# Kernel optimization log

Measured on AMD Instinct MI355X. Metric: run time of the kernel, lower is better.

Reference implementation:

```python
import jax, jax.numpy as jnp
import numpy as np

B, S, D, H = 2, 2048, 1024, 16
DK = D // H  # 64
SQRT_DK = DK ** 0.5
NEG = -1e9


def setup_inputs() -> dict:
    key = jax.random.key(0)
    ks = jax.random.split(key, 7)
    scale = 1.0 / np.sqrt(D)
    return {
        "x": jax.random.normal(ks[0], (B, S, D), jnp.float32),
        "encoder_output": jax.random.normal(ks[1], (B, S, D), jnp.float32),
        "mask": jax.random.randint(ks[2], (B, S), 0, 2, jnp.int32),
        "WQ": jax.random.normal(ks[3], (D, D), jnp.float32) * scale,
        "WK": jax.random.normal(ks[4], (D, D), jnp.float32) * scale,
        "WV": jax.random.normal(ks[5], (D, D), jnp.float32) * scale,
        "WO": jax.random.normal(ks[6], (D, D), jnp.float32) * scale,
    }


def reference(x, encoder_output, mask, WQ, WK, WV, WO):
    b, s, d = x.shape
    # project and split heads: (b, h, s, dk)
    q = (x @ WQ).reshape(b, s, H, DK).transpose(0, 2, 1, 3)
    k = (encoder_output @ WK).reshape(b, s, H, DK).transpose(0, 2, 1, 3)
    v = (encoder_output @ WV).reshape(b, s, H, DK).transpose(0, 2, 1, 3)
    # scores: (b, h, s_q, s_k)
    scores = jnp.einsum('bhqd,bhkd->bhqk', q, k) / SQRT_DK
    # future mask (strict upper triangle) + padding mask broadcast over key dim
    future = jnp.triu(jnp.ones((s, s), jnp.int32), 1)  # (s, s)
    m = mask[:, None, :, None] + future[None, None, :, :]  # (b, 1->h, s_q, s_k)
    scores = jnp.where(m != 0, NEG, scores)
    attn = jax.nn.softmax(scores, axis=-1)
    # context: (b, s, h, dk) -> (b, s, d)
    ctx = jnp.einsum('bhqk,bhkd->bqhd', attn, v).reshape(b, s, d)
    return ctx @ WO
```

## Files before the change

### kernel.cpp

```cpp
#include <hip/hip_runtime.h>
#include <hip/hip_bf16.h>

constexpr int B = 2, S = 2048, D = 1024, H = 16, DK = 64;
constexpr int M = B * S;
constexpr float LOG2E = 1.44269504088896f;
constexpr float NEGBIG = -3.0e38f;
constexpr float QSCALE = 0.125f * LOG2E;

using short8 = __attribute__((ext_vector_type(8))) short;
using short4v = __attribute__((ext_vector_type(4))) short;
using f32x4 = __attribute__((ext_vector_type(4))) float;

#define GLOBAL_AS __attribute__((address_space(1)))
#define LDS_AS __attribute__((address_space(3)))

__device__ __forceinline__ void gll16(const void* g, void* l) {
  __builtin_amdgcn_global_load_lds((const GLOBAL_AS void*)g, (LDS_AS void*)l, 16, 0, 0);
}

__device__ __forceinline__ short f2bf(float f) {
  __hip_bfloat16 h = __float2bfloat16(f);
  short s;
  __builtin_memcpy(&s, &h, 2);
  return s;
}
__device__ __forceinline__ unsigned pack2bf(float a, float b) {
  return (unsigned)(unsigned short)f2bf(a) | ((unsigned)(unsigned short)f2bf(b) << 16);
}

__global__ __launch_bounds__(256) void prep_kernel(const float* __restrict__ x,
                                                   const float* __restrict__ enc,
                                                   const float* __restrict__ W0,
                                                   const float* __restrict__ W1,
                                                   const float* __restrict__ W2,
                                                   const float* __restrict__ W3,
                                                   short* __restrict__ xb,
                                                   short* __restrict__ encb,
                                                   short* __restrict__ Wt) {
  __shared__ float t[64][65];
  const int bx = blockIdx.x;
  if (bx < 8192) {
    const float4* src = (const float4*)((bx & 4096) ? enc : x);
    short4v* dst = (short4v*)((bx & 4096) ? encb : xb);
    const int i = (bx & 4095) * 256 + threadIdx.x;
    const float4 v = src[i];
    short4v o;
    o[0] = f2bf(v.x); o[1] = f2bf(v.y); o[2] = f2bf(v.z); o[3] = f2bf(v.w);
    dst[i] = o;
  } else {
    const int idx = bx - 8192;
    const int z = idx >> 8, rem = idx & 255;
    const float* W = z == 0 ? W0 : z == 1 ? W1 : z == 2 ? W2 : W3;
    short* dstw = Wt + (size_t)z * D * D;
    const int n0 = (rem & 15) * 64, k0 = (rem >> 4) * 64;
    const int lx = threadIdx.x & 63, ly = threadIdx.x >> 6;
    #pragma unroll
    for (int r = 0; r < 64; r += 4)
      t[r + ly][lx] = W[(size_t)(k0 + r + ly) * D + n0 + lx];
    __syncthreads();
    #pragma unroll
    for (int r = 0; r < 64; r += 4)
      dstw[(size_t)(n0 + r + ly) * D + k0 + lx] = f2bf(t[lx][r + ly]);
  }
}

__global__ __launch_bounds__(512, 2) void gemm_qkv_kernel(const short* __restrict__ A0,
                                                          const short* __restrict__ A1,
                                                          const short* __restrict__ Wts,
                                                          short* __restrict__ Cv,
                                                          float* __restrict__ vsum) {
  __shared__ char AsL[65536];
  __shared__ char BsL[65536];
  const int z = blockIdx.z;
  const short* __restrict__ A = z ? A1 : A0;
  const short* __restrict__ Bt = Wts + (size_t)z * D * D;
  const float oscale = (z == 0) ? QSCALE : 1.0f;

  const int tid = threadIdx.x;
  const int lane = tid & 63, wid = tid >> 6;
  const int l15 = lane & 15, lg = lane >> 4;
  const int row0 = blockIdx.x * 256, col0 = blockIdx.y * 256;
  const int wm = wid >> 2, wn = wid & 3;
  f32x4 acc[8][4] = {};

  auto stageH = [&](int mat, int sbuf, int half, int tile) {
    const short* src = mat ? Bt : A;
    const int base0 = mat ? col0 : row0;
    char* dst = (mat ? BsL : AsL) + sbuf * 32768 + half * 16384;
    const int k0 = tile * 64;
    #pragma unroll
    for (int it = 0; it < 2; ++it) {
      const int c = tid + it * 512;
      const int row = c & 127, kc = c >> 7;
      gll16(&src[(size_t)(base0 + half * 128 + row) * D + k0 + kc * 8],
            dst + kc * 2048 + row * 16);
    }
  };

#define PHASE(RBUF, MH, NH, DOSTAGE, SMAT, SBUF, SH, STILE, VM)                            \
  do {                                                                                     \
    short8 af_[4][2], bv_[2][2];                                                           \
    const char* ab_ = AsL + (RBUF) * 32768 + (MH) * 16384;                                 \
    const char* bb_ = BsL + (RBUF) * 32768 + (NH) * 16384;                                 \
    _Pragma("unroll") for (int m16 = 0; m16 < 4; ++m16)                                    \
        _Pragma("unroll") for (int ks = 0; ks < 2; ++ks)                                   \
            af_[m16][ks] = *(const short8*)(ab_ + (ks * 4 + lg) * 2048 +                   \
                                            (wm * 64 + m16 * 16 + l15) * 16);              \
    _Pragma("unroll") for (int n16 = 0; n16 < 2; ++n16)                                    \
        _Pragma("unroll") for (int ks = 0; ks < 2; ++ks)                                   \
            bv_[n16][ks] = *(const short8*)(bb_ + (ks * 4 + lg) * 2048 +                   \
                                            (wn * 32 + n16 * 16 + l15) * 16);              \
    if (DOSTAGE) stageH((SMAT), (SBUF), (SH), (STILE));                                    \
    __builtin_amdgcn_s_barrier();                                                          \
    asm volatile("s_waitcnt lgkmcnt(0)" ::: "memory");                                     \
    __builtin_amdgcn_sched_barrier(0);                                                     \
    __builtin_amdgcn_s_setprio(1);                                                         \
    _Pragma("unroll") for (int m16 = 0; m16 < 4; ++m16)                                    \
        _Pragma("unroll") for (int n16 = 0; n16 < 2; ++n16)                                \
            _Pragma("unroll") for (int ks = 0; ks < 2; ++ks)                               \
                acc[(MH) * 4 + m16][(NH) * 2 + n16] =                                      \
                    __builtin_amdgcn_mfma_f32_16x16x32_bf16(                               \
                        af_[m16][ks], bv_[n16][ks], acc[(MH) * 4 + m16][(NH) * 2 + n16],   \
                        0, 0, 0);                                                          \
    __builtin_amdgcn_s_setprio(0);                                                         \
    if ((VM) == 4) asm volatile("s_waitcnt vmcnt(4)" ::: "memory");                        \
    else if ((VM) == 0) asm volatile("s_waitcnt vmcnt(0)" ::: "memory");                   \
    __builtin_amdgcn_s_barrier();                                                          \
    __builtin_amdgcn_sched_barrier(0);                                                     \
  } while (0)

  stageH(0, 0, 0, 0);
  stageH(1, 0, 0, 0);
  stageH(0, 0, 1, 0);
  stageH(1, 0, 1, 0);
  stageH(0, 1, 0, 1);
  stageH(1, 1, 0, 1);
  asm volatile("s_waitcnt vmcnt(4)" ::: "memory");
  __builtin_amdgcn_s_barrier();
  __builtin_amdgcn_sched_barrier(0);

  #pragma unroll 1
  for (int i = 0; i < 8; ++i) {
    const int tb = 2 * i + 1, ta2 = 2 * i + 2, tb2 = 2 * i + 3;
    const bool pre = (i < 7);
    const int vm = pre ? 4 : 0;
    PHASE(0, 0, 0, true, 0, 1, 1, tb, -1);
    PHASE(0, 0, 1, true, 1, 1, 1, tb, -1);
    PHASE(0, 1, 0, pre, 0, 0, 0, ta2, -1);
    PHASE(0, 1, 1, pre, 1, 0, 0, ta2, vm);
    PHASE(1, 0, 0, pre, 0, 0, 1, ta2, -1);
    PHASE(1, 0, 1, pre, 1, 0, 1, ta2, -1);
    PHASE(1, 1, 0, pre, 0, 1, 0, tb2, -1);
    PHASE(1, 1, 1, pre, 1, 1, 0, tb2, vm);
  }
#undef PHASE

  #pragma unroll
  for (int mh = 0; mh < 2; ++mh)
    #pragma unroll
    for (int m16 = 0; m16 < 4; ++m16)
      #pragma unroll
      for (int r = 0; r < 4; ++r) {
        const int row = row0 + mh * 128 + wm * 64 + m16 * 16 + 4 * lg + r;
        #pragma unroll
        for (int nh = 0; nh < 2; ++nh)
          #pragma unroll
          for (int n16 = 0; n16 < 2; ++n16) {
            const int col = col0 + nh * 128 + wn * 32 + n16 * 16 + l15;
            Cv[(size_t)z * M * D + (size_t)row * D + col] =
                f2bf(acc[mh * 4 + m16][nh * 2 + n16][r] * oscale);
          }
      }
  if (z == 2) {
    const int bidx = row0 >> 11;
    #pragma unroll
    for (int nh = 0; nh < 2; ++nh)
      #pragma unroll
      for (int n16 = 0; n16 < 2; ++n16) {
        float s = 0.f;
        #pragma unroll
        for (int mh = 0; mh < 2; ++mh)
          #pragma unroll
          for (int m16 = 0; m16 < 4; ++m16) {
            const f32x4 a4 = acc[mh * 4 + m16][nh * 2 + n16];
            s += a4[0] + a4[1] + a4[2] + a4[3];
          }
        s += __shfl_xor(s, 16);
        s += __shfl_xor(s, 32);
        if (lg == 0)
          atomicAdd(&vsum[(size_t)bidx * D + col0 + nh * 128 + wn * 32 + n16 * 16 + l15], s);
      }
  }
}

__global__ __launch_bounds__(256) void gemmO_kernel(const short* __restrict__ A,
                                                    const short* __restrict__ Bt,
                                                    float* __restrict__ C) {
  __shared__ short As[2][4][128][8];
  __shared__ short Bs[2][4][64][8];
  const int tid = threadIdx.x;
  const int lane = tid & 63, wid = tid >> 6;
  const int l15 = lane & 15, lg = lane >> 4;
  const int row0 = blockIdx.x * 128, col0 = blockIdx.y * 64;
  const int wm = wid >> 1, wn = wid & 1;
  f32x4 acc[4][2] = {};

  auto stage = [&](int k0, int nb) {
    #pragma unroll
    for (int it = 0; it < 2; ++it) {
      const int c = tid + it * 256;
      const int row = c & 127, kc2 = c >> 7;
      gll16(&A[(size_t)(row0 + row) * D + k0 + kc2 * 8],
            (char*)As + nb * 8192 + (wid * 64 + it * 256) * 16);
    }
    gll16(&Bt[(size_t)(col0 + lane) * D + k0 + wid * 8],
          (char*)Bs + nb * 4096 + wid * 1024);
  };

  stage(0, 0);
  __syncthreads();
  int cur = 0;
  for (int t = 0; t < D / 32; ++t) {
    if (t < D / 32 - 1) stage((t + 1) * 32, cur ^ 1);
    short8 af[4], bfr[2];
    #pragma unroll
    for (int m = 0; m < 4; ++m) af[m] = *(const short8*)&As[cur][lg][wm * 64 + m * 16 + l15][0];
    #pragma unroll
    for (int n = 0; n < 2; ++n) bfr[n] = *(const short8*)&Bs[cur][lg][wn * 32 + n * 16 + l15][0];
    #pragma unroll
    for (int m = 0; m < 4; ++m)
      #pragma unroll
      for (int n = 0; n < 2; ++n)
        acc[m][n] = __builtin_amdgcn_mfma_f32_16x16x32_bf16(af[m], bfr[n], acc[m][n], 0, 0, 0);
    __syncthreads();
    cur ^= 1;
  }
  #pragma unroll
  for (int m = 0; m < 4; ++m)
    #pragma unroll
    for (int r = 0; r < 4; ++r) {
      const int row = row0 + wm * 64 + m * 16 + 4 * lg + r;
      #pragma unroll
      for (int n = 0; n < 2; ++n)
        C[(size_t)row * D + col0 + wn * 32 + n * 16 + l15] = acc[m][n][r];
    }
}

__device__ __forceinline__ int keyof(int c, int i) {
  return ((c >> 1) << 5) + ((i >> 2) << 3) + ((c & 1) << 2) + (i & 3);
}
__device__ __forceinline__ int vt_byte(int kc, int d, int ksb) {
  return kc * 1024 + ((d ^ (kc & 7)) << 4) + ksb * 2;
}

__global__ __launch_bounds__(512, 4) void attn_kernel(const short* __restrict__ Qb,
                                                      const short* __restrict__ Kb,
                                                      const short* __restrict__ Vb,
                                                      const int* __restrict__ maskp,
                                                      const float* __restrict__ vsum,
                                                      short* __restrict__ ctxb) {
  __shared__ char KsBuf[2][16384];
  __shared__ char VtBuf[2][16384];
  const int bid = blockIdx.x;
  const int qt = (bid < 256) ? 15 - (bid >> 5) : (bid >> 5) - 8;
  const int bh = bid & 31;
  const int b = bh >> 4, h = bh & 15;
  const int tid = threadIdx.x, lane = tid & 63, wid = tid >> 6;
  const int l15 = lane & 15, lg = lane >> 4;
  const int ql = wid * 16 + l15;

  short8 qf[2];
  {
    const size_t o = (size_t)(b * S + qt * 128 + ql) * D + h * DK;
    qf[0] = *(const short8*)&Qb[o + lg * 8];
    qf[1] = *(const short8*)&Qb[o + 32 + lg * 8];
  }
  f32x4 cx[4] = {};
  f32x4 cl = {};
  short8 ones8;
  #pragma unroll
  for (int j = 0; j < 8; ++j) ones8[j] = (short)0x3F80;

  const int kkey = keyof(lg, l15);
  const int vu = tid & 63, dv = tid >> 6;
  const int vh = vu >> 5, vl = vu & 31;
  const int vkc = vl >> 2, vksb = (vl & 3) * 2;

  auto stageK = [&](int jc, int nb) {
    const size_t base = (size_t)(b * S + jc * 128 + kkey) * D + h * DK + wid * 8;
    gll16(&Kb[base], (char*)KsBuf + nb * 16384 + wid * 1024);
    gll16(&Kb[base + (size_t)64 * D], (char*)KsBuf + nb * 16384 + 8192 + wid * 1024);
  };
  auto loadV = [&](int jc, short8& va, short8& vb2) {
    const size_t vb0 = (size_t)(b * S + jc * 128 + 2 * vu) * D + h * DK + dv * 8;
    va = *(const short8*)&Vb[vb0];
    vb2 = *(const short8*)&Vb[vb0 + D];
  };
  auto writeV = [&](int nb, const short8& va, const short8& vb2) {
    char* dst = (char*)VtBuf + nb * 16384 + vh * 8192;
    #pragma unroll
    for (int i = 0; i < 8; ++i) {
      const unsigned w = (unsigned)(unsigned short)va[i] | ((unsigned)(unsigned short)vb2[i] << 16);
      *(unsigned*)(dst + vt_byte(vkc, dv * 8 + i, vksb)) = w;
    }
  };

  auto tile_pair = [&](int nb, bool do1, bool mask0, bool mask1) {
    const char* ks0 = (const char*)KsBuf + nb * 16384;
    const char* ks1 = ks0 + 8192;
    const char* vt0 = (const char*)VtBuf + nb * 16384;
    const char* vt1 = vt0 + 8192;
    f32x4 sa0[4], sa1[4];
    #pragma unroll
    for (int c = 0; c < 4; ++c) {
      const short8 kf0 = *(const short8*)(ks0 + lg * 1024 + c * 256 + l15 * 16);
      const short8 kf1 = *(const short8*)(ks0 + (4 + lg) * 1024 + c * 256 + l15 * 16);
      f32x4 zz = {0.f, 0.f, 0.f, 0.f};
      zz = __builtin_amdgcn_mfma_f32_16x16x32_bf16(kf0, qf[0], zz, 0, 0, 0);
      zz = __builtin_amdgcn_mfma_f32_16x16x32_bf16(kf1, qf[1], zz, 0, 0, 0);
      sa0[c] = zz;
    }
    if (do1) {
      #pragma unroll
      for (int c = 0; c < 4; ++c) {
        const short8 kf0 = *(const short8*)(ks1 + lg * 1024 + c * 256 + l15 * 16);
        const short8 kf1 = *(const short8*)(ks1 + (4 + lg) * 1024 + c * 256 + l15 * 16);
        f32x4 zz = {0.f, 0.f, 0.f, 0.f};
        zz = __builtin_amdgcn_mfma_f32_16x16x32_bf16(kf0, qf[0], zz, 0, 0, 0);
        zz = __builtin_amdgcn_mfma_f32_16x16x32_bf16(kf1, qf[1], zz, 0, 0, 0);
        sa1[c] = zz;
      }
    }
    if (mask0) {
      #pragma unroll
      for (int c = 0; c < 4; ++c)
        #pragma unroll
        for (int r = 0; r < 4; ++r)
          if (((c >> 1) << 5) + (lg << 3) + ((c & 1) << 2) + r > ql) sa0[c][r] = NEGBIG;
    }
    if (do1 && mask1) {
      #pragma unroll
      for (int c = 0; c < 4; ++c)
        #pragma unroll
        for (int r = 0; r < 4; ++r)
          if (64 + ((c >> 1) << 5) + (lg << 3) + ((c & 1) << 2) + r > ql) sa1[c][r] = NEGBIG;
    }
    {
      short8 pf[2];
      #pragma unroll
      for (int kk = 0; kk < 2; ++kk)
        #pragma unroll
        for (int jj = 0; jj < 8; ++jj)
          pf[kk][jj] = f2bf(exp2f(sa0[kk * 2 + (jj >> 2)][jj & 3]));
      #pragma unroll
      for (int kk = 0; kk < 2; ++kk) {
        #pragma unroll
        for (int dt = 0; dt < 4; ++dt) {
          const short8 vf = *(const short8*)(vt0 + vt_byte(kk * 4 + lg, dt * 16 + l15, 0));
          cx[dt] = __builtin_amdgcn_mfma_f32_16x16x32_bf16(vf, pf[kk], cx[dt], 0, 0, 0);
        }
        cl = __builtin_amdgcn_mfma_f32_16x16x32_bf16(ones8, pf[kk], cl, 0, 0, 0);
      }
    }
    if (do1) {
      short8 pf[2];
      #pragma unroll
      for (int kk = 0; kk < 2; ++kk)
        #pragma unroll
        for (int jj = 0; jj < 8; ++jj)
          pf[kk][jj] = f2bf(exp2f(sa1[kk * 2 + (jj >> 2)][jj & 3]));
      #pragma unroll
      for (int kk = 0; kk < 2; ++kk) {
        #pragma unroll
        for (int dt = 0; dt < 4; ++dt) {
          const short8 vf = *(const short8*)(vt1 + vt_byte(kk * 4 + lg, dt * 16 + l15, 0));
          cx[dt] = __builtin_amdgcn_mfma_f32_16x16x32_bf16(vf, pf[kk], cx[dt], 0, 0, 0);
        }
        cl = __builtin_amdgcn_mfma_f32_16x16x32_bf16(ones8, pf[kk], cl, 0, 0, 0);
      }
    }
  };

  {
    short8 va, vb2;
    stageK(0, 0);
    loadV(0, va, vb2);
    writeV(0, va, vb2);
  }
  __syncthreads();
  int cur = 0;
  for (int jc = 0; jc <= qt; ++jc) {
    short8 nva, nvb;
    if (jc < qt) { stageK(jc + 1, cur ^ 1); loadV(jc + 1, nva, nvb); }
    const bool diag = (jc == qt), hi = (wid >= 4);
    tile_pair(cur, !diag || hi, diag && !hi, diag && hi);
    if (jc < qt) writeV(cur ^ 1, nva, nvb);
    __syncthreads();
    cur ^= 1;
  }

  {
    const int qg = qt * 128 + ql;
    const int mq = maskp[b * S + qg];
    const float inv = 1.0f / cl[0];
    constexpr float vscale = 1.0f / S;
    short* orow = &ctxb[(size_t)(b * S + qg) * D + h * DK];
    const float* vmb = &vsum[(size_t)b * D + h * DK];
    #pragma unroll
    for (int dt = 0; dt < 4; ++dt)
      #pragma unroll
      for (int p2 = 0; p2 < 2; ++p2) {
        const int d = dt * 16 + 4 * lg + p2 * 2;
        const float v0 = mq ? vmb[d] * vscale     : cx[dt][p2 * 2] * inv;
        const float v1 = mq ? vmb[d + 1] * vscale : cx[dt][p2 * 2 + 1] * inv;
        *(unsigned*)&orow[d] = pack2bf(v0, v1);
      }
  }
}

extern "C" void kernel_launch(void* const* d_in, const int* in_sizes, int n_in,
                              void* d_out, int out_size, void* d_ws, size_t ws_size,
                              hipStream_t stream) {
  (void)in_sizes; (void)n_in; (void)out_size; (void)ws_size;
  const float* x   = (const float*)d_in[0];
  const float* enc = (const float*)d_in[1];
  const int*   msk = (const int*)d_in[2];
  const float* WQ  = (const float*)d_in[3];
  const float* WK  = (const float*)d_in[4];
  const float* WV  = (const float*)d_in[5];
  const float* WO  = (const float*)d_in[6];
  float* out = (float*)d_out;

  char* ws = (char*)d_ws;
  const size_t MB = 1u << 20;
  short* xb    = (short*)(ws + 0);
  short* encb  = (short*)(ws + 8 * MB);
  short* Qb    = (short*)(ws + 16 * MB);
  short* WQt   = (short*)(ws + 40 * MB);
  float* vsum  = (float*)(ws + 48 * MB);
  short* Kb    = Qb + (size_t)M * D;
  short* Vb    = Kb + (size_t)M * D;
  short* WOt   = WQt + (size_t)3 * D * D;
  short* ctxb  = xb;

  hipMemsetAsync(vsum, 0, (size_t)B * D * sizeof(float), stream);

  prep_kernel<<<dim3(9216), 256, 0, stream>>>(x, enc, WQ, WK, WV, WO, xb, encb, WQt);

  gemm_qkv_kernel<<<dim3(M / 256, D / 256, 3), 512, 0, stream>>>(xb, encb, WQt, Qb, vsum);

  attn_kernel<<<dim3(512), 512, 0, stream>>>(Qb, Kb, Vb, msk, vsum, ctxb);

  gemmO_kernel<<<dim3(M / 128, D / 64), 256, 0, stream>>>(ctxb, WOt, out);
}
```

Measured before the change: 152.1 us.

## Split long causal attention rows across two blocks and merge partials in combine kernel

Query tiles 8-15 of the causal attention now have their key ranges split across two blocks, driven by a static schedule table. Each block writes unnormalized bf16 partial context and row sums, and a new combine kernel adds the halves, normalizes and applies the padding mask. Other changes: V goes to a single LDS buffer with extra barriers, occupancy is raised to 6 blocks per CU, and MFMA sections get s_setprio hints. The aim is balanced load across 768 blocks, at the cost of an extra launch, partial-result traffic, and bf16 rounding of the unnormalized partials.

```diff
diff --git a/kernel.cpp b/kernel.cpp
--- a/kernel.cpp
+++ b/kernel.cpp
@@ -24,9 +24,18 @@
   __builtin_memcpy(&s, &h, 2);
   return s;
 }
+__device__ __forceinline__ float bf2f(short s) {
+  __hip_bfloat16 h;
+  __builtin_memcpy(&h, &s, 2);
+  return __bfloat162float(h);
+}
 __device__ __forceinline__ unsigned pack2bf(float a, float b) {
   return (unsigned)(unsigned short)f2bf(a) | ((unsigned)(unsigned short)f2bf(b) << 16);
 }
+
+__constant__ int QT_D[24] = {15,14, 7,13,13,12, 6,10,  15,14,12,11,11,10, 9, 5,   0, 1, 2, 8, 3, 9, 8, 4};
+__constant__ int J0_D[24] = { 0, 0, 0, 0, 7, 0, 0, 0,   8, 8, 7, 0, 6, 6, 5, 0,   0, 0, 0, 5, 0, 0, 0, 0};
+__constant__ int J1_D[24] = { 8, 8, 8, 7,14, 7, 7, 6,  16,15,13, 6,12,11,10, 6,   1, 2, 3, 9, 4, 5, 5, 5};
 
 __global__ __launch_bounds__(256) void prep_kernel(const float* __restrict__ x,
                                                    const float* __restrict__ enc,
@@ -253,17 +262,21 @@
   return kc * 1024 + ((d ^ (kc & 7)) << 4) + ksb * 2;
 }
 
-__global__ __launch_bounds__(512, 4) void attn_kernel(const short* __restrict__ Qb,
+__global__ __launch_bounds__(512, 6) void attn_kernel(const short* __restrict__ Qb,
                                                       const short* __restrict__ Kb,
                                                       const short* __restrict__ Vb,
                                                       const int* __restrict__ maskp,
                                                       const float* __restrict__ vsum,
-                                                      short* __restrict__ ctxb) {
+                                                      short* __restrict__ ctxb,
+                                                      short* __restrict__ pctx0,
+                                                      short* __restrict__ pctx1,
+                                                      float* __restrict__ pl0,
+                                                      float* __restrict__ pl1) {
   __shared__ char KsBuf[2][16384];
-  __shared__ char VtBuf[2][16384];
+  __shared__ char VtS[16384];
   const int bid = blockIdx.x;
-  const int qt = (bid < 256) ? 15 - (bid >> 5) : (bid >> 5) - 8;
-  const int bh = bid & 31;
+  const int didx = bid >> 5, bh = bid & 31;
+  const int qt = QT_D[didx], j0 = J0_D[didx], j1 = J1_D[didx];
   const int b = bh >> 4, h = bh & 15;
   const int tid = threadIdx.x, lane = tid & 63, wid = tid >> 6;
   const int l15 = lane & 15, lg = lane >> 4;
@@ -286,18 +299,18 @@
   const int vh = vu >> 5, vl = vu & 31;
   const int vkc = vl >> 2, vksb = (vl & 3) * 2;
 
-  auto stageK = [&](int jc, int nb) {
+  auto stageK = [&](int jc, int kb) {
     const size_t base = (size_t)(b * S + jc * 128 + kkey) * D + h * DK + wid * 8;
-    gll16(&Kb[base], (char*)KsBuf + nb * 16384 + wid * 1024);
-    gll16(&Kb[base + (size_t)64 * D], (char*)KsBuf + nb * 16384 + 8192 + wid * 1024);
+    gll16(&Kb[base], (char*)KsBuf + kb * 16384 + wid * 1024);
+    gll16(&Kb[base + (size_t)64 * D], (char*)KsBuf + kb * 16384 + 8192 + wid * 1024);
   };
   auto loadV = [&](int jc, short8& va, short8& vb2) {
     const size_t vb0 = (size_t)(b * S + jc * 128 + 2 * vu) * D + h * DK + dv * 8;
     va = *(const short8*)&Vb[vb0];
     vb2 = *(const short8*)&Vb[vb0 + D];
   };
-  auto writeV = [&](int nb, const short8& va, const short8& vb2) {
-    char* dst = (char*)VtBuf + nb * 16384 + vh * 8192;
+  auto writeV = [&](const short8& va, const short8& vb2) {
+    char* dst = (char*)VtS + vh * 8192;
     #pragma unroll
     for (int i = 0; i < 8; ++i) {
       const unsigned w = (unsigned)(unsigned short)va[i] | ((unsigned)(unsigned short)vb2[i] << 16);
@@ -305,12 +318,13 @@
     }
   };
 
-  auto tile_pair = [&](int nb, bool do1, bool mask0, bool mask1) {
-    const char* ks0 = (const char*)KsBuf + nb * 16384;
+  auto tile_pair = [&](int kb, bool do1, bool mask0, bool mask1) {
+    const char* ks0 = (const char*)KsBuf + kb * 16384;
     const char* ks1 = ks0 + 8192;
-    const char* vt0 = (const char*)VtBuf + nb * 16384;
+    const char* vt0 = (const char*)VtS;
     const char* vt1 = vt0 + 8192;
     f32x4 sa0[4], sa1[4];
+    __builtin_amdgcn_s_setprio(1);
     #pragma unroll
     for (int c = 0; c < 4; ++c) {
       const short8 kf0 = *(const short8*)(ks0 + lg * 1024 + c * 256 + l15 * 16);
@@ -331,6 +345,7 @@
         sa1[c] = zz;
       }
     }
+    __builtin_amdgcn_s_setprio(0);
     if (mask0) {
       #pragma unroll
       for (int c = 0; c < 4; ++c)
@@ -352,6 +367,7 @@
         #pragma unroll
         for (int jj = 0; jj < 8; ++jj)
           pf[kk][jj] = f2bf(exp2f(sa0[kk * 2 + (jj >> 2)][jj & 3]));
+      __builtin_amdgcn_s_setprio(1);
       #pragma unroll
       for (int kk = 0; kk < 2; ++kk) {
         #pragma unroll
@@ -361,6 +377,7 @@
         }
         cl = __builtin_amdgcn_mfma_f32_16x16x32_bf16(ones8, pf[kk], cl, 0, 0, 0);
       }
+      __builtin_amdgcn_s_setprio(0);
     }
     if (do1) {
       short8 pf[2];
@@ -369,6 +386,7 @@
         #pragma unroll
         for (int jj = 0; jj < 8; ++jj)
           pf[kk][jj] = f2bf(exp2f(sa1[kk * 2 + (jj >> 2)][jj & 3]));
+      __builtin_amdgcn_s_setprio(1);
       #pragma unroll
       for (int kk = 0; kk < 2; ++kk) {
         #pragma unroll
@@ -378,28 +396,33 @@
         }
         cl = __builtin_amdgcn_mfma_f32_16x16x32_bf16(ones8, pf[kk], cl, 0, 0, 0);
       }
+      __builtin_amdgcn_s_setprio(0);
     }
   };
 
   {
     short8 va, vb2;
-    stageK(0, 0);
-    loadV(0, va, vb2);
-    writeV(0, va, vb2);
-  }
-  __syncthreads();
-  int cur = 0;
-  for (int jc = 0; jc <= qt; ++jc) {
+    stageK(j0, 0);
+    loadV(j0, va, vb2);
+    writeV(va, vb2);
+    asm volatile("s_waitcnt vmcnt(0) lgkmcnt(0)" ::: "memory");
+    __builtin_amdgcn_s_barrier();
+  }
+  int kb = 0;
+  for (int jc = j0; jc < j1; ++jc) {
     short8 nva, nvb;
-    if (jc < qt) { stageK(jc + 1, cur ^ 1); loadV(jc + 1, nva, nvb); }
+    const bool hasnext = (jc + 1 < j1);
+    if (hasnext) { loadV(jc + 1, nva, nvb); stageK(jc + 1, kb ^ 1); }
     const bool diag = (jc == qt), hi = (wid >= 4);
-    tile_pair(cur, !diag || hi, diag && !hi, diag && hi);
-    if (jc < qt) writeV(cur ^ 1, nva, nvb);
-    __syncthreads();
-    cur ^= 1;
-  }
-
-  {
+    tile_pair(kb, !diag || hi, diag && !hi, diag && hi);
+    __builtin_amdgcn_s_barrier();
+    if (hasnext) writeV(nva, nvb);
+    asm volatile("s_waitcnt vmcnt(0) lgkmcnt(0)" ::: "memory");
+    __builtin_amdgcn_s_barrier();
+    kb ^= 1;
+  }
+
+  if (qt < 8) {
     const int qg = qt * 128 + ql;
     const int mq = maskp[b * S + qg];
     const float inv = 1.0f / cl[0];
@@ -415,6 +438,49 @@
         const float v1 = mq ? vmb[d + 1] * vscale : cx[dt][p2 * 2 + 1] * inv;
         *(unsigned*)&orow[d] = pack2bf(v0, v1);
       }
+  } else {
+    const int part = (j0 != 0);
+    short* pc = (part ? pctx1 : pctx0) + ((((size_t)bh * 8 + (qt - 8)) * 128 + ql) * 64);
+    float* plp = (part ? pl1 : pl0);
+    #pragma unroll
+    for (int dt = 0; dt < 4; ++dt) {
+      *(unsigned*)&pc[dt * 16 + 4 * lg]     = pack2bf(cx[dt][0], cx[dt][1]);
+      *(unsigned*)&pc[dt * 16 + 4 * lg + 2] = pack2bf(cx[dt][2], cx[dt][3]);
+    }
+    if (lg == 0) plp[((size_t)bh * 8 + (qt - 8)) * 128 + ql] = cl[0];
+  }
+}
+
+__global__ __launch_bounds__(256) void combine_kernel(const short* __restrict__ pctx0,
+                                                      const short* __restrict__ pctx1,
+                                                      const float* __restrict__ pl0,
+                                                      const float* __restrict__ pl1,
+                                                      const int* __restrict__ maskp,
+                                                      const float* __restrict__ vsum,
+                                                      short* __restrict__ ctxb) {
+  const int qt8 = blockIdx.x, bh = blockIdx.y;
+  const int b = bh >> 4, h = bh & 15;
+  const int qt = 8 + qt8;
+  const int t = threadIdx.x;
+  const int row = t >> 1, dh = (t & 1) * 32;
+  const size_t rbase = ((size_t)bh * 8 + qt8) * 128 + row;
+  const float inv = 1.0f / (pl0[rbase] + pl1[rbase]);
+  const int qg = qt * 128 + row;
+  const int mq = maskp[b * S + qg];
+  constexpr float vscale = 1.0f / S;
+  short* orow = &ctxb[(size_t)(b * S + qg) * D + h * DK + dh];
+  const float* vmb = &vsum[(size_t)b * D + h * DK + dh];
+  const unsigned* u0 = (const unsigned*)(pctx0 + rbase * 64 + dh);
+  const unsigned* u1 = (const unsigned*)(pctx1 + rbase * 64 + dh);
+  #pragma unroll
+  for (int i = 0; i < 16; ++i) {
+    const unsigned a = u0[i], c = u1[i];
+    const float s0 = bf2f((short)(a & 0xffff)) + bf2f((short)(c & 0xffff));
+    const float s1 = bf2f((short)(a >> 16)) + bf2f((short)(c >> 16));
+    const int d = 2 * i;
+    const float v0 = mq ? vmb[d] * vscale     : s0 * inv;
+    const float v1 = mq ? vmb[d + 1] * vscale : s1 * inv;
+    *(unsigned*)&orow[d] = pack2bf(v0, v1);
   }
 }
 
@@ -438,10 +504,14 @@
   short* Qb    = (short*)(ws + 16 * MB);
   short* WQt   = (short*)(ws + 40 * MB);
   float* vsum  = (float*)(ws + 48 * MB);
+  float* pl0   = (float*)(ws + 48 * MB + 16 * 1024);
+  float* pl1   = pl0 + 32 * 8 * 128;
   short* Kb    = Qb + (size_t)M * D;
   short* Vb    = Kb + (size_t)M * D;
   short* WOt   = WQt + (size_t)3 * D * D;
   short* ctxb  = xb;
+  short* pctx0 = encb;
+  short* pctx1 = encb + (size_t)2 * MB;
 
   hipMemsetAsync(vsum, 0, (size_t)B * D * sizeof(float), stream);
 
@@ -449,7 +519,10 @@
 
   gemm_qkv_kernel<<<dim3(M / 256, D / 256, 3), 512, 0, stream>>>(xb, encb, WQt, Qb, vsum);
 
-  attn_kernel<<<dim3(512), 512, 0, stream>>>(Qb, Kb, Vb, msk, vsum, ctxb);
+  attn_kernel<<<dim3(768), 512, 0, stream>>>(Qb, Kb, Vb, msk, vsum, ctxb,
+                                             pctx0, pctx1, pl0, pl1);
+
+  combine_kernel<<<dim3(8, 32), 256, 0, stream>>>(pctx0, pctx1, pl0, pl1, msk, vsum, ctxb);
 
   gemmO_kernel<<<dim3(M / 128, D / 64), 256, 0, stream>>>(ctxb, WOt, out);
 }
```

Result: slower. 198.9 us (+30.8%).
